# Optimization experiments

Hardware: AMD Instinct MI355X
Metric: run time of the kernel (lower is better)

The kernel has to match this reference:

```python
import jax, jax.numpy as jnp
import numpy as np

N_NODES = 50000
N_EDGES = 800000
IN_DIM = 128
HIDDEN = 64
HEADS = 4
OUT_DIM = 64
NEG_SLOPE = 0.2


def setup_inputs() -> dict:
    key = jax.random.key(0)
    ks = jax.random.split(key, 16)
    def lin(k, fan_in, fan_out):
        return jax.random.normal(k, (fan_in, fan_out), dtype=jnp.float32) * (1.0 / np.sqrt(fan_in))
    def attn(k):
        return jax.random.normal(k, (HEADS, HIDDEN), dtype=jnp.float32) * 0.1
    inp = {
        "x": jax.random.normal(ks[0], (N_NODES, IN_DIM), dtype=jnp.float32),
        "src": jax.random.randint(ks[1], (N_EDGES,), 0, N_NODES, dtype=jnp.int32),
        "dst": jax.random.randint(ks[2], (N_EDGES,), 0, N_NODES, dtype=jnp.int32),
        # layer 0: in_dim -> heads*hidden
        "W0": lin(ks[3], IN_DIM, HEADS * HIDDEN),
        "al0": attn(ks[4]),
        "ar0": attn(ks[5]),
        # layer 1: heads*hidden -> heads*hidden
        "W1": lin(ks[6], HEADS * HIDDEN, HEADS * HIDDEN),
        "al1": attn(ks[7]),
        "ar1": attn(ks[8]),
        # final layer: heads*hidden -> heads*out_dim
        "W2": lin(ks[9], HEADS * HIDDEN, HEADS * OUT_DIM),
        "al2": jax.random.normal(ks[10], (HEADS, OUT_DIM), dtype=jnp.float32) * 0.1,
        "ar2": jax.random.normal(ks[11], (HEADS, OUT_DIM), dtype=jnp.float32) * 0.1,
        # output head: out_dim -> 1
        "Wout": lin(ks[12], OUT_DIM, 1),
        "bout": jnp.zeros((1,), dtype=jnp.float32),
    }
    return inp


def gat_layer(x, src, dst, W, al, ar):
    """DGL-style multi-head graph attention conv (edge gather/softmax/aggregate)."""
    N = x.shape[0]
    H, D = al.shape
    h = (x @ W).reshape(N, H, D)                      # [N,H,D]
    el = jnp.sum(h * al, axis=-1)                     # [N,H]
    er = jnp.sum(h * ar, axis=-1)                     # [N,H]
    e = jax.nn.leaky_relu(el[src] + er[dst], NEG_SLOPE)   # [E,H]
    # numerically-stable edge softmax segmented by destination node
    m = jax.ops.segment_max(e, dst, num_segments=N)   # [N,H]
    m = jnp.where(jnp.isfinite(m), m, 0.0)
    ex = jnp.exp(e - m[dst])                          # [E,H]
    denom = jax.ops.segment_sum(ex, dst, num_segments=N)  # [N,H]
    alpha = ex / (denom[dst] + 1e-9)                  # [E,H]
    msg = h[src] * alpha[..., None]                   # [E,H,D] (dominant traffic)
    out = jax.ops.segment_sum(msg, dst, num_segments=N)   # [N,H,D]
    return jax.nn.elu(out)


def reference(x, src, dst, W0, al0, ar0, W1, al1, ar1, W2, al2, ar2, Wout, bout):
    N = x.shape[0]
    # layer 0 (threshold layer also produces node index split index1/index0)
    h = gat_layer(x, src, dst, W0, al0, ar0)          # [N,H,HID]
    h = h.reshape(N, -1)                              # flatten(start=1,end=2)
    # middle layer
    h = gat_layer(h, src, dst, W1, al1, ar1)
    h = h.reshape(N, -1)
    # final layer + head-mean pool
    feats = gat_layer(h, src, dst, W2, al2, ar2)      # [N,H,OUT]
    feats = feats.mean(axis=1)                        # [N,OUT]
    out = jax.nn.relu(feats @ Wout + bout)            # [N,1]
    return out
```

## Files before the change

### kernel.cpp

```cpp
#include <hip/hip_runtime.h>
#include <hip/hip_fp16.h>
#include <math.h>

#define NN 50000
#define NE 800000
#define HEADS 4
#define HID 64
#define HD 256
#define NEG_SLOPE 0.2f

typedef __attribute__((ext_vector_type(8))) short short8;
typedef __attribute__((ext_vector_type(4))) float f32x4;
typedef __attribute__((ext_vector_type(2))) unsigned int uint2v;

__device__ __forceinline__ unsigned short f2bf(float f) {
    unsigned u = __float_as_uint(f);
    u += 0x7fff + ((u >> 16) & 1);
    return (unsigned short)(u >> 16);
}
__device__ __forceinline__ float bf2f(unsigned short b) {
    return __uint_as_float(((unsigned)b) << 16);
}

__device__ __forceinline__ float h2f_bits(unsigned short b) {
    __half_raw r; r.x = b;
    return __half2float(__half(r));
}
__device__ __forceinline__ unsigned short f2h_bits(float f) {
    __half_raw r(__float2half(f));
    return r.x;
}

__device__ __forceinline__ void wsplit_one(const float* W, unsigned short* Wf, int idx) {
    int lane = idx & 63;
    int tile = (idx >> 6) & 15;
    int kb   = idx >> 10;
    int col  = tile * 16 + (lane & 15);
    int krow = kb * 32 + (lane >> 4) * 8;
    unsigned short* p = Wf + ((size_t)(kb * 16 + tile) * 2 * 64 + lane) * 8;
#pragma unroll
    for (int j = 0; j < 8; j++) {
        float v = W[(size_t)(krow + j) * HD + col];
        unsigned short h = f2bf(v);
        unsigned short l = f2bf(v - bf2f(h));
        p[j] = h;
        p[512 + j] = l;
    }
}

__global__ __launch_bounds__(256) void prep_count_kernel(
    const float* __restrict__ W0, unsigned short* __restrict__ Wf0,
    const float* __restrict__ W1, unsigned short* __restrict__ Wf1,
    const float* __restrict__ W2, unsigned short* __restrict__ Wf2,
    const int* __restrict__ dst, int* __restrict__ cnt) {
    int b = (int)blockIdx.x;
    if (b < 80) {
        int idx = b * 256 + (int)threadIdx.x;
        const int n0 = 4 * 16 * 64;
        const int n1 = 8 * 16 * 64;
        if (idx < n0) wsplit_one(W0, Wf0, idx);
        else if (idx < n0 + n1) wsplit_one(W1, Wf1, idx - n0);
        else if (idx < n0 + 2 * n1) wsplit_one(W2, Wf2, idx - n0 - n1);
    } else {
        int e = ((b - 80) * 256 + (int)threadIdx.x) * 2;
        if (e + 1 < NE) {
            int2 d = *(const int2*)&dst[e];
            atomicAdd(&cnt[d.x], 1);
            atomicAdd(&cnt[d.y], 1);
        } else if (e < NE) {
            atomicAdd(&cnt[dst[e]], 1);
        }
    }
}

__global__ __launch_bounds__(1024) void rowptr_kernel(
    const int* __restrict__ cnt, int* __restrict__ rowptr,
    int* __restrict__ cursor, int n) {
    __shared__ int wsum[16];
    __shared__ int csum_s[16];
    int t = (int)threadIdx.x;
    int base = (int)blockIdx.x * 1024;
    int idx = base + t;
    int lane = t & 63, wid = t >> 6;

    int v = (idx < n) ? cnt[idx] : 0;

    int cp = 0;
    for (int j = t; j < base; j += 1024) cp += cnt[j];

    int x = v;
#pragma unroll
    for (int off = 1; off < 64; off <<= 1) {
        int y = __shfl_up(x, off);
        if (lane >= off) x += y;
    }
#pragma unroll
    for (int off = 32; off > 0; off >>= 1) cp += __shfl_down(cp, off);
    if (lane == 63) wsum[wid] = x;
    if (lane == 0) csum_s[wid] = cp;
    __syncthreads();

    if (t < 16) {
        int wv = wsum[t];
#pragma unroll
        for (int off = 1; off < 16; off <<= 1) {
            int y = __shfl_up(wv, off);
            if (t >= off) wv += y;
        }
        wsum[t] = wv;
    } else if (wid == 1) {
        int cv = (lane < 16) ? csum_s[lane] : 0;
#pragma unroll
        for (int off = 32; off > 0; off >>= 1) cv += __shfl_down(cv, off);
        if (lane == 0) csum_s[0] = cv;
    }
    __syncthreads();

    int waveOff = wid ? wsum[wid - 1] : 0;
    int chunkOff = csum_s[0];
    int incl = x + waveOff + chunkOff;
    int excl = incl - v;
    if (idx < n) { rowptr[idx] = excl; cursor[idx] = excl; }
    if (idx == n - 1) rowptr[n] = incl;
}

template <int K, int F32A>
__device__ __forceinline__ void mfma_gemm_body(
    int bid,
    const ushort* __restrict__ Xh, const ushort* __restrict__ Xl,
    const float* __restrict__ Xf,
    const unsigned short* __restrict__ Wf,
    ushort* __restrict__ H,
    const float* __restrict__ al, const float* __restrict__ ar,
    float* __restrict__ el, float* __restrict__ er,
    ushort* ldsA) {
    constexpr int KB = K / 32;
    int tid = (int)threadIdx.x;
    int w = tid >> 6;
    int lane = tid & 63;
    int rowBase = bid * 64;
    int mrow = lane & 15;
    int q = lane >> 4;

    f32x4 acc[4][4];
#pragma unroll
    for (int r = 0; r < 4; r++)
#pragma unroll
        for (int c = 0; c < 4; c++) {
            f32x4 z = {0.f, 0.f, 0.f, 0.f};
            acc[r][c] = z;
        }

    int srow = tid >> 2, qq = tid & 3;
    int grow = rowBase + srow;
    grow = grow < NN ? grow : NN - 1;
    int sr = srow >> 4, smrow = srow & 15;
    int flane = qq * 16 + smrow;
    ushort* sHi = &ldsA[((size_t)(sr * 2 + 0) * 64 + flane) * 8];

    short8 rh0, rl0, rh1, rl1;
    float4 rf00, rf01, rf10, rf11;

    auto loadA0 = [&](int kb) {
        if constexpr (F32A) {
            const float* xp = Xf + (size_t)grow * K + kb * 32 + qq * 8;
            rf00 = *(const float4*)xp;
            rf01 = *(const float4*)(xp + 4);
        } else {
            rh0 = *(const short8*)(Xh + (size_t)grow * K + kb * 32 + qq * 8);
            rl0 = *(const short8*)(Xl + (size_t)grow * K + kb * 32 + qq * 8);
        }
    };
    auto loadA1 = [&](int kb) {
        if constexpr (F32A) {
            const float* xp = Xf + (size_t)grow * K + kb * 32 + qq * 8;
            rf10 = *(const float4*)xp;
            rf11 = *(const float4*)(xp + 4);
        } else {
            rh1 = *(const short8*)(Xh + (size_t)grow * K + kb * 32 + qq * 8);
            rl1 = *(const short8*)(Xl + (size_t)grow * K + kb * 32 + qq * 8);
        }
    };
    auto cvt8 = [&](float4 a, float4 b, short8& h8, short8& l8) {
        float vv[8] = {a.x, a.y, a.z, a.w, b.x, b.y, b.z, b.w};
#pragma unroll
        for (int j = 0; j < 8; j++) {
            unsigned short hh = f2bf(vv[j]);
            h8[j] = (short)hh;
            l8[j] = (short)f2bf(vv[j] - bf2f(hh));
        }
    };
    auto storeA0 = [&]() {
        if constexpr (F32A) {
            short8 h8, l8;
            cvt8(rf00, rf01, h8, l8);
            *(short8*)sHi = h8;
            *(short8*)(sHi + 512) = l8;
        } else {
            *(short8*)sHi = rh0;
            *(short8*)(sHi + 512) = rl0;
        }
    };
    auto storeA1 = [&]() {
        if constexpr (F32A) {
            short8 h8, l8;
            cvt8(rf10, rf11, h8, l8);
            *(short8*)(sHi + 4096) = h8;
            *(short8*)(sHi + 4096 + 512) = l8;
        } else {
            *(short8*)(sHi + 4096) = rh1;
            *(short8*)(sHi + 4096 + 512) = rl1;
        }
    };

    auto compute = [&](int kb, int pofs) {
        short8 Wh[4], Wl_[4];
#pragma unroll
        for (int c = 0; c < 4; c++) {
            const unsigned short* wp =
                Wf + (((size_t)(kb * 16 + w * 4 + c) * 2) * 64 + lane) * 8;
            Wh[c]  = *(const short8*)wp;
            Wl_[c] = *(const short8*)(wp + 512);
        }
        short8 Ah[4], Al_[4];
#pragma unroll
        for (int r = 0; r < 4; r++) {
            Ah[r]  = *(const short8*)&ldsA[pofs + ((r * 2 + 0) * 64 + lane) * 8];
            Al_[r] = *(const short8*)&ldsA[pofs + ((r * 2 + 1) * 64 + lane) * 8];
        }
#pragma unroll
        for (int c = 0; c < 4; c++)
#pragma unroll
            for (int r = 0; r < 4; r++) {
                acc[r][c] = __builtin_amdgcn_mfma_f32_16x16x32_bf16(Ah[r],  Wh[c],  acc[r][c], 0, 0, 0);
                acc[r][c] = __builtin_amdgcn_mfma_f32_16x16x32_bf16(Ah[r],  Wl_[c], acc[r][c], 0, 0, 0);
                acc[r][c] = __builtin_amdgcn_mfma_f32_16x16x32_bf16(Al_[r], Wh[c],  acc[r][c], 0, 0, 0);
            }
    };

    loadA0(0);
    loadA1(1);
    for (int kb = 0; kb < KB; kb += 2) {
        __syncthreads();
        storeA0();
        storeA1();
        __syncthreads();
        if (kb + 2 < KB) {
            loadA0(kb + 2);
            loadA1(kb + 3);
        }
        compute(kb, 0);
        compute(kb + 1, 4096);
    }

    int n0 = w * 64;
    float alv[4], arv[4];
#pragma unroll
    for (int c = 0; c < 4; c++) {
        alv[c] = al[n0 + c * 16 + mrow];
        arv[c] = ar[n0 + c * 16 + mrow];
    }
#pragma unroll
    for (int r = 0; r < 4; r++) {
        float pl[4] = {0.f, 0.f, 0.f, 0.f};
        float pr[4] = {0.f, 0.f, 0.f, 0.f};
#pragma unroll
        for (int c = 0; c < 4; c++)
#pragma unroll
            for (int g = 0; g < 4; g++) {
                pl[g] += acc[r][c][g] * alv[c];
                pr[g] += acc[r][c][g] * arv[c];
            }
#pragma unroll
        for (int g = 0; g < 4; g++) {
#pragma unroll
            for (int off = 1; off < 16; off <<= 1) {
                pl[g] += __shfl_xor(pl[g], off);
                pr[g] += __shfl_xor(pr[g], off);
            }
        }
#pragma unroll
        for (int g = 0; g < 4; g++) {
            int row = rowBase + r * 16 + q * 4 + g;
            if (row < NN) {
#pragma unroll
                for (int c = 0; c < 4; c++)
                    H[(size_t)row * HD + n0 + c * 16 + mrow] = f2h_bits(acc[r][c][g]);
                if (mrow == 0) {
                    el[row * 4 + w] = pl[g];
                    er[row * 4 + w] = pr[g];
                }
            }
        }
    }
}

template <int K, int F32A>
__global__ __launch_bounds__(256, 3) void mfma_gemm_kernel(
    const ushort* __restrict__ Xh, const ushort* __restrict__ Xl,
    const float* __restrict__ Xf,
    const unsigned short* __restrict__ Wf,
    ushort* __restrict__ H,
    const float* __restrict__ al, const float* __restrict__ ar,
    float* __restrict__ el, float* __restrict__ er) {
    __shared__ ushort ldsA[2 * 8 * 64 * 8];
    mfma_gemm_body<K, F32A>((int)blockIdx.x, Xh, Xl, Xf, Wf, H, al, ar, el, er, ldsA);
}

__global__ __launch_bounds__(256, 3) void gemm0_scatter_kernel(
    const float* __restrict__ Xf, const unsigned short* __restrict__ Wf,
    ushort* __restrict__ H,
    const float* __restrict__ al, const float* __restrict__ ar,
    float* __restrict__ el, float* __restrict__ er,
    const int* __restrict__ src, const int* __restrict__ dst,
    int* __restrict__ cursor, int* __restrict__ csr_src) {
    __shared__ ushort ldsA[2 * 8 * 64 * 8];
    int b = (int)blockIdx.x;
    int g = b / 5, rem = b % 5;
    if (rem == 0) {
        mfma_gemm_body<128, 1>(g, nullptr, nullptr, Xf, Wf, H, al, ar, el, er, ldsA);
    } else {
        int e = (g * 4 + (rem - 1)) * 256 + (int)threadIdx.x;
        if (e < NE) {
            int p = atomicAdd(&cursor[dst[e]], 1);
            csr_src[p] = src[e];
        }
    }
}

__device__ __forceinline__ float lrelu(float x) { return fmaxf(x, NEG_SLOPE * x); }

__device__ __forceinline__ float4 us4tof4(ushort4 u) {
    float4 f;
    f.x = h2f_bits(u.x); f.y = h2f_bits(u.y);
    f.z = h2f_bits(u.z); f.w = h2f_bits(u.w);
    return f;
}

template <int FINAL>
__global__ __launch_bounds__(256) void gat_node_kernel(
    const ushort* __restrict__ H, const float* __restrict__ el, const float* __restrict__ er,
    const int* __restrict__ rowptr, const int* __restrict__ csr_src,
    ushort* __restrict__ out_hi, ushort* __restrict__ out_lo,
    const float* __restrict__ Wout, const float* __restrict__ bout,
    float* __restrict__ final_out) {
    int wave = threadIdx.x >> 6, lane = threadIdx.x & 63;
    int v = blockIdx.x * 4 + wave;
    if (v >= NN) return;
    int beg = rowptr[v], end = rowptr[v + 1];

    int hh = lane >> 4;
    float er_h = er[v * 4 + hh];
    const float* elh = el + hh;
    unsigned lane4 = (unsigned)(lane * 4);

    float ss0 = 0.f, ss1 = 0.f, ss2 = 0.f, ss3 = 0.f;
    float4 a0 = make_float4(0.f, 0.f, 0.f, 0.f);
    float4 a1 = make_float4(0.f, 0.f, 0.f, 0.f);
    float4 a2 = make_float4(0.f, 0.f, 0.f, 0.f);
    float4 a3 = make_float4(0.f, 0.f, 0.f, 0.f);
    {
        int i = beg;
        for (; i + 4 <= end; i += 4) {
            unsigned s0 = (unsigned)csr_src[i];
            unsigned s1 = (unsigned)csr_src[i + 1];
            unsigned s2 = (unsigned)csr_src[i + 2];
            unsigned s3 = (unsigned)csr_src[i + 3];
            ushort4 q0 = *(const ushort4*)(H + ((s0 << 8) + lane4));
            ushort4 q1 = *(const ushort4*)(H + ((s1 << 8) + lane4));
            ushort4 q2 = *(const ushort4*)(H + ((s2 << 8) + lane4));
            ushort4 q3 = *(const ushort4*)(H + ((s3 << 8) + lane4));
            float w0 = __expf(lrelu(elh[s0 * 4u] + er_h));
            float w1 = __expf(lrelu(elh[s1 * 4u] + er_h));
            float w2 = __expf(lrelu(elh[s2 * 4u] + er_h));
            float w3 = __expf(lrelu(elh[s3 * 4u] + er_h));
            float4 h0 = us4tof4(q0);
            float4 h1 = us4tof4(q1);
            float4 h2 = us4tof4(q2);
            float4 h3 = us4tof4(q3);
            ss0 += w0; ss1 += w1; ss2 += w2; ss3 += w3;
            a0.x += w0 * h0.x; a0.y += w0 * h0.y; a0.z += w0 * h0.z; a0.w += w0 * h0.w;
            a1.x += w1 * h1.x; a1.y += w1 * h1.y; a1.z += w1 * h1.z; a1.w += w1 * h1.w;
            a2.x += w2 * h2.x; a2.y += w2 * h2.y; a2.z += w2 * h2.z; a2.w += w2 * h2.w;
            a3.x += w3 * h3.x; a3.y += w3 * h3.y; a3.z += w3 * h3.z; a3.w += w3 * h3.w;
        }
        for (; i < end; i++) {
            unsigned s0 = (unsigned)csr_src[i];
            ushort4 q0 = *(const ushort4*)(H + ((s0 << 8) + lane4));
            float w0 = __expf(lrelu(elh[s0 * 4u] + er_h));
            float4 h0 = us4tof4(q0);
            ss0 += w0;
            a0.x += w0 * h0.x; a0.y += w0 * h0.y; a0.z += w0 * h0.z; a0.w += w0 * h0.w;
        }
    }
    float ssum = (ss0 + ss1) + (ss2 + ss3);
    float4 acc;
    acc.x = (a0.x + a1.x) + (a2.x + a3.x);
    acc.y = (a0.y + a1.y) + (a2.y + a3.y);
    acc.z = (a0.z + a1.z) + (a2.z + a3.z);
    acc.w = (a0.w + a1.w) + (a2.w + a3.w);

    float inv = 1.0f / (ssum + 1e-9f);
    acc.x *= inv; acc.y *= inv; acc.z *= inv; acc.w *= inv;

    acc.x = acc.x > 0.f ? acc.x : expm1f(acc.x);
    acc.y = acc.y > 0.f ? acc.y : expm1f(acc.y);
    acc.z = acc.z > 0.f ? acc.z : expm1f(acc.z);
    acc.w = acc.w > 0.f ? acc.w : expm1f(acc.w);

    if (!FINAL) {
        ushort4 hv, lv;
        hv.x = f2bf(acc.x); lv.x = f2bf(acc.x - bf2f(hv.x));
        hv.y = f2bf(acc.y); lv.y = f2bf(acc.y - bf2f(hv.y));
        hv.z = f2bf(acc.z); lv.z = f2bf(acc.z - bf2f(hv.z));
        hv.w = f2bf(acc.w); lv.w = f2bf(acc.w - bf2f(hv.w));
        uint2v ph = { (unsigned)hv.x | ((unsigned)hv.y << 16),
                      (unsigned)hv.z | ((unsigned)hv.w << 16) };
        uint2v pl = { (unsigned)lv.x | ((unsigned)lv.y << 16),
                      (unsigned)lv.z | ((unsigned)lv.w << 16) };
        __builtin_nontemporal_store(ph, (uint2v*)(out_hi + (size_t)v * HD + lane * 4));
        __builtin_nontemporal_store(pl, (uint2v*)(out_lo + (size_t)v * HD + lane * 4));
    } else {
        acc.x += __shfl_xor(acc.x, 16); acc.x += __shfl_xor(acc.x, 32);
        acc.y += __shfl_xor(acc.y, 16); acc.y += __shfl_xor(acc.y, 32);
        acc.z += __shfl_xor(acc.z, 16); acc.z += __shfl_xor(acc.z, 32);
        acc.w += __shfl_xor(acc.w, 16); acc.w += __shfl_xor(acc.w, 32);
        float4 w4 = *(const float4*)&Wout[(lane & 15) * 4];
        float p = 0.25f * (acc.x * w4.x + acc.y * w4.y + acc.z * w4.z + acc.w * w4.w);
        p += __shfl_xor(p, 1);
        p += __shfl_xor(p, 2);
        p += __shfl_xor(p, 4);
        p += __shfl_xor(p, 8);
        if (lane == 0) final_out[v] = fmaxf(p + bout[0], 0.f);
    }
}

extern "C" void kernel_launch(void* const* d_in, const int* in_sizes, int n_in,
                              void* d_out, int out_size, void* d_ws, size_t ws_size,
                              hipStream_t stream) {
    const float* x    = (const float*)d_in[0];
    const int*   src  = (const int*)d_in[1];
    const int*   dst  = (const int*)d_in[2];
    const float* W0   = (const float*)d_in[3];
    const float* al0  = (const float*)d_in[4];
    const float* ar0  = (const float*)d_in[5];
    const float* W1   = (const float*)d_in[6];
    const float* al1  = (const float*)d_in[7];
    const float* ar1  = (const float*)d_in[8];
    const float* W2   = (const float*)d_in[9];
    const float* al2  = (const float*)d_in[10];
    const float* ar2  = (const float*)d_in[11];
    const float* Wout = (const float*)d_in[12];
    const float* bout = (const float*)d_in[13];
    float* outp = (float*)d_out;

    char* ws = (char*)d_ws;
    size_t off = 0;
    auto carve = [&](size_t n) -> char* {
        char* p = ws + off;
        off += (n + 255) & ~(size_t)255;
        return p;
    };
    ushort* h_buf  = (ushort*)carve((size_t)NN * HD * 2);
    ushort* xh     = (ushort*)carve((size_t)NN * HD * 2);
    ushort* xl     = (ushort*)carve((size_t)NN * HD * 2);
    float*  el     = (float*)carve((size_t)NN * HEADS * 4);
    float*  er     = (float*)carve((size_t)NN * HEADS * 4);
    int*    cnt    = (int*)carve((size_t)NN * 4);
    int*    cursor = (int*)carve((size_t)NN * 4);
    int*    rowptr = (int*)carve((size_t)(NN + 1) * 4);
    int*    csr_src= (int*)carve((size_t)NE * 4);
    unsigned short* Wf0 = (unsigned short*)carve((size_t)4 * 16 * 64 * 16 * 2);
    unsigned short* Wf1 = (unsigned short*)carve((size_t)8 * 16 * 64 * 16 * 2);
    unsigned short* Wf2 = (unsigned short*)carve((size_t)8 * 16 * 64 * 16 * 2);

    const int nCountBlk = (NE / 2 + 255) / 256;
    const int gGemm = (NN + 63) / 64;
    const int gNode = (NN + 3) / 4;
    const int NCH = (NN + 1023) / 1024;

    hipMemsetAsync(cnt, 0, (size_t)NN * 4, stream);
    prep_count_kernel<<<80 + nCountBlk, 256, 0, stream>>>(W0, Wf0, W1, Wf1, W2, Wf2, dst, cnt);
    rowptr_kernel<<<NCH, 1024, 0, stream>>>(cnt, rowptr, cursor, NN);
    gemm0_scatter_kernel<<<gGemm * 5, 256, 0, stream>>>(
        x, Wf0, h_buf, al0, ar0, el, er, src, dst, cursor, csr_src);
    gat_node_kernel<0><<<gNode, 256, 0, stream>>>(h_buf, el, er, rowptr, csr_src,
                                                  xh, xl, nullptr, nullptr, nullptr);
    mfma_gemm_kernel<256, 0><<<gGemm, 256, 0, stream>>>(xh, xl, nullptr, Wf1,
                                                        h_buf, al1, ar1, el, er);
    gat_node_kernel<0><<<gNode, 256, 0, stream>>>(h_buf, el, er, rowptr, csr_src,
                                                  xh, xl, nullptr, nullptr, nullptr);
    mfma_gemm_kernel<256, 0><<<gGemm, 256, 0, stream>>>(xh, xl, nullptr, Wf2,
                                                        h_buf, al2, ar2, el, er);
    gat_node_kernel<1><<<gNode, 256, 0, stream>>>(h_buf, el, er, rowptr, csr_src,
                                                  nullptr, nullptr, Wout, bout, outp);
}
```

Measured before the change: 451.1 us.

## Stage full-K activation tile in LDS once for layer-1/2 GEMMs

Replaces the double-buffered K-loop GEMM for the 256-wide hidden layers with a kernel that loads the whole 64x256 hi/lo bf16 activation tile into LDS up front, syncs once, then runs all K steps without further barriers. This removes the per-iteration syncthreads and the register staging of the loop. In exchange the block uses 64 KB of LDS and more registers, so occupancy drops (launch bounds changes from 3 to 2 blocks) and load latency is no longer overlapped with compute. The shared epilogue is factored into a helper.

```diff
diff --git a/kernel.cpp b/kernel.cpp
--- a/kernel.cpp
+++ b/kernel.cpp
@@ -124,16 +124,61 @@
     if (idx == n - 1) rowptr[n] = incl;
 }
 
-template <int K, int F32A>
-__device__ __forceinline__ void mfma_gemm_body(
+__device__ __forceinline__ void gemm_epilogue(
+    f32x4 (&acc)[4][4], int rowBase, int w, int mrow, int q,
+    ushort* __restrict__ H, const float* __restrict__ al, const float* __restrict__ ar,
+    float* __restrict__ el, float* __restrict__ er) {
+    int n0 = w * 64;
+    float alv[4], arv[4];
+#pragma unroll
+    for (int c = 0; c < 4; c++) {
+        alv[c] = al[n0 + c * 16 + mrow];
+        arv[c] = ar[n0 + c * 16 + mrow];
+    }
+#pragma unroll
+    for (int r = 0; r < 4; r++) {
+        float pl[4] = {0.f, 0.f, 0.f, 0.f};
+        float pr[4] = {0.f, 0.f, 0.f, 0.f};
+#pragma unroll
+        for (int c = 0; c < 4; c++)
+#pragma unroll
+            for (int g = 0; g < 4; g++) {
+                pl[g] += acc[r][c][g] * alv[c];
+                pr[g] += acc[r][c][g] * arv[c];
+            }
+#pragma unroll
+        for (int g = 0; g < 4; g++) {
+#pragma unroll
+            for (int off = 1; off < 16; off <<= 1) {
+                pl[g] += __shfl_xor(pl[g], off);
+                pr[g] += __shfl_xor(pr[g], off);
+            }
+        }
+#pragma unroll
+        for (int g = 0; g < 4; g++) {
+            int row = rowBase + r * 16 + q * 4 + g;
+            if (row < NN) {
+#pragma unroll
+                for (int c = 0; c < 4; c++)
+                    H[(size_t)row * HD + n0 + c * 16 + mrow] = f2h_bits(acc[r][c][g]);
+                if (mrow == 0) {
+                    el[row * 4 + w] = pl[g];
+                    er[row * 4 + w] = pr[g];
+                }
+            }
+        }
+    }
+}
+
+__device__ __forceinline__ void mfma_gemm_body_f32(
     int bid,
-    const ushort* __restrict__ Xh, const ushort* __restrict__ Xl,
     const float* __restrict__ Xf,
     const unsigned short* __restrict__ Wf,
     ushort* __restrict__ H,
     const float* __restrict__ al, const float* __restrict__ ar,
     float* __restrict__ el, float* __restrict__ er,
     ushort* ldsA) {
+    constexpr int K = 128;
     constexpr int KB = K / 32;
     int tid = (int)threadIdx.x;
     int w = tid >> 6;
@@ -158,28 +203,17 @@
     int flane = qq * 16 + smrow;
     ushort* sHi = &ldsA[((size_t)(sr * 2 + 0) * 64 + flane) * 8];
 
-    short8 rh0, rl0, rh1, rl1;
     float4 rf00, rf01, rf10, rf11;
 
     auto loadA0 = [&](int kb) {
-        if constexpr (F32A) {
-            const float* xp = Xf + (size_t)grow * K + kb * 32 + qq * 8;
-            rf00 = *(const float4*)xp;
-            rf01 = *(const float4*)(xp + 4);
-        } else {
-            rh0 = *(const short8*)(Xh + (size_t)grow * K + kb * 32 + qq * 8);
-            rl0 = *(const short8*)(Xl + (size_t)grow * K + kb * 32 + qq * 8);
-        }
+        const float* xp = Xf + (size_t)grow * K + kb * 32 + qq * 8;
+        rf00 = *(const float4*)xp;
+        rf01 = *(const float4*)(xp + 4);
     };
     auto loadA1 = [&](int kb) {
-        if constexpr (F32A) {
-            const float* xp = Xf + (size_t)grow * K + kb * 32 + qq * 8;
-            rf10 = *(const float4*)xp;
-            rf11 = *(const float4*)(xp + 4);
-        } else {
-            rh1 = *(const short8*)(Xh + (size_t)grow * K + kb * 32 + qq * 8);
-            rl1 = *(const short8*)(Xl + (size_t)grow * K + kb * 32 + qq * 8);
-        }
+        const float* xp = Xf + (size_t)grow * K + kb * 32 + qq * 8;
+        rf10 = *(const float4*)xp;
+        rf11 = *(const float4*)(xp + 4);
     };
     auto cvt8 = [&](float4 a, float4 b, short8& h8, short8& l8) {
         float vv[8] = {a.x, a.y, a.z, a.w, b.x, b.y, b.z, b.w};
@@ -191,26 +225,16 @@
         }
     };
     auto storeA0 = [&]() {
-        if constexpr (F32A) {
-            short8 h8, l8;
-            cvt8(rf00, rf01, h8, l8);
-            *(short8*)sHi = h8;
-            *(short8*)(sHi + 512) = l8;
-        } else {
-            *(short8*)sHi = rh0;
-            *(short8*)(sHi + 512) = rl0;
-        }
+        short8 h8, l8;
+        cvt8(rf00, rf01, h8, l8);
+        *(short8*)sHi = h8;
+        *(short8*)(sHi + 512) = l8;
     };
     auto storeA1 = [&]() {
-        if constexpr (F32A) {
-            short8 h8, l8;
-            cvt8(rf10, rf11, h8, l8);
-            *(short8*)(sHi + 4096) = h8;
-            *(short8*)(sHi + 4096 + 512) = l8;
-        } else {
-            *(short8*)(sHi + 4096) = rh1;
-            *(short8*)(sHi + 4096 + 512) = rl1;
-        }
+        short8 h8, l8;
+        cvt8(rf10, rf11, h8, l8);
+        *(short8*)(sHi + 4096) = h8;
+        *(short8*)(sHi + 4096 + 512) = l8;
     };
 
     auto compute = [&](int kb, int pofs) {
@@ -253,58 +277,7 @@
         compute(kb + 1, 4096);
     }
 
-    int n0 = w * 64;
-    float alv[4], arv[4];
-#pragma unroll
-    for (int c = 0; c < 4; c++) {
-        alv[c] = al[n0 + c * 16 + mrow];
-        arv[c] = ar[n0 + c * 16 + mrow];
-    }
-#pragma unroll
-    for (int r = 0; r < 4; r++) {
-        float pl[4] = {0.f, 0.f, 0.f, 0.f};
-        float pr[4] = {0.f, 0.f, 0.f, 0.f};
-#pragma unroll
-        for (int c = 0; c < 4; c++)
-#pragma unroll
-            for (int g = 0; g < 4; g++) {
-                pl[g] += acc[r][c][g] * alv[c];
-                pr[g] += acc[r][c][g] * arv[c];
-            }
-#pragma unroll
-        for (int g = 0; g < 4; g++) {
-#pragma unroll
-            for (int off = 1; off < 16; off <<= 1) {
-                pl[g] += __shfl_xor(pl[g], off);
-                pr[g] += __shfl_xor(pr[g], off);
-            }
-        }
-#pragma unroll
-        for (int g = 0; g < 4; g++) {
-            int row = rowBase + r * 16 + q * 4 + g;
-            if (row < NN) {
-#pragma unroll
-                for (int c = 0; c < 4; c++)
-                    H[(size_t)row * HD + n0 + c * 16 + mrow] = f2h_bits(acc[r][c][g]);
-                if (mrow == 0) {
-                    el[row * 4 + w] = pl[g];
-                    er[row * 4 + w] = pr[g];
-                }
-            }
-        }
-    }
-}
-
-template <int K, int F32A>
-__global__ __launch_bounds__(256, 3) void mfma_gemm_kernel(
-    const ushort* __restrict__ Xh, const ushort* __restrict__ Xl,
-    const float* __restrict__ Xf,
-    const unsigned short* __restrict__ Wf,
-    ushort* __restrict__ H,
-    const float* __restrict__ al, const float* __restrict__ ar,
-    float* __restrict__ el, float* __restrict__ er) {
-    __shared__ ushort ldsA[2 * 8 * 64 * 8];
-    mfma_gemm_body<K, F32A>((int)blockIdx.x, Xh, Xl, Xf, Wf, H, al, ar, el, er, ldsA);
+    gemm_epilogue(acc, rowBase, w, mrow, q, H, al, ar, el, er);
 }
 
 __global__ __launch_bounds__(256, 3) void gemm0_scatter_kernel(
@@ -318,7 +291,7 @@
     int b = (int)blockIdx.x;
     int g = b / 5, rem = b % 5;
     if (rem == 0) {
-        mfma_gemm_body<128, 1>(g, nullptr, nullptr, Xf, Wf, H, al, ar, el, er, ldsA);
+        mfma_gemm_body_f32(g, Xf, Wf, H, al, ar, el, er, ldsA);
     } else {
         int e = (g * 4 + (rem - 1)) * 256 + (int)threadIdx.x;
         if (e < NE) {
@@ -326,6 +299,81 @@
             csr_src[p] = src[e];
         }
     }
+}
+
+__global__ __launch_bounds__(256, 2) void mfma_gemm_fullk_kernel(
+    const ushort* __restrict__ Xh, const ushort* __restrict__ Xl,
+    const unsigned short* __restrict__ Wf,
+    ushort* __restrict__ H,
+    const float* __restrict__ al, const float* __restrict__ ar,
+    float* __restrict__ el, float* __restrict__ er) {
+    constexpr int K = 256;
+    constexpr int KB = K / 32;
+    __shared__ ushort ldsA[KB * 4 * 2 * 64 * 8];
+    int tid = (int)threadIdx.x;
+    int w = tid >> 6;
+    int lane = tid & 63;
+    int rowBase = (int)blockIdx.x * 64;
+    int mrow = lane & 15;
+    int q = lane >> 4;
+
+    int srow = tid >> 2, qq = tid & 3;
+    int grow = rowBase + srow;
+    grow = grow < NN ? grow : NN - 1;
+    int sr = srow >> 4, smrow = srow & 15;
+    int flane = qq * 16 + smrow;
+    const ushort* xhp = Xh + (size_t)grow * K + qq * 8;
+    const ushort* xlp = Xl + (size_t)grow * K + qq * 8;
+
+    short8 sh[KB], sl[KB];
+#pragma unroll
+    for (int kb = 0; kb < KB; kb++) {
+        sh[kb] = *(const short8*)(xhp + kb * 32);
+        sl[kb] = *(const short8*)(xlp + kb * 32);
+    }
+#pragma unroll
+    for (int kb = 0; kb < KB; kb++) {
+        *(short8*)&ldsA[((size_t)(kb * 8 + sr * 2 + 0) * 64 + flane) * 8] = sh[kb];
+        *(short8*)&ldsA[((size_t)(kb * 8 + sr * 2 + 1) * 64 + flane) * 8] = sl[kb];
+    }
+    __syncthreads();
+
+    f32x4 acc[4][4];
+#pragma unroll
+    for (int r = 0; r < 4; r++)
+#pragma unroll
+        for (int c = 0; c < 4; c++) {
+            f32x4 z = {0.f, 0.f, 0.f, 0.f};
+            acc[r][c] = z;
+        }
+
+    for (int kb = 0; kb < KB; kb++) {
+        const ushort* Abase = &ldsA[(size_t)kb * 8 * 512];
+        short8 Wh[4], Wl_[4];
+#pragma unroll
+        for (int c = 0; c < 4; c++) {
+            const unsigned short* wp =
+                Wf + (((size_t)(kb * 16 + w * 4 + c) * 2) * 64 + lane) * 8;
+            Wh[c]  = *(const short8*)wp;
+            Wl_[c] = *(const short8*)(wp + 512);
+        }
+        short8 Ah[4], Al_[4];
+#pragma unroll
+        for (int r = 0; r < 4; r++) {
+            Ah[r]  = *(const short8*)&Abase[((r * 2 + 0) * 64 + lane) * 8];
+            Al_[r] = *(const short8*)&Abase[((r * 2 + 1) * 64 + lane) * 8];
+        }
+#pragma unroll
+        for (int c = 0; c < 4; c++)
+#pragma unroll
+            for (int r = 0; r < 4; r++) {
+                acc[r][c] = __builtin_amdgcn_mfma_f32_16x16x32_bf16(Ah[r],  Wh[c],  acc[r][c], 0, 0, 0);
+                acc[r][c] = __builtin_amdgcn_mfma_f32_16x16x32_bf16(Ah[r],  Wl_[c], acc[r][c], 0, 0, 0);
+                acc[r][c] = __builtin_amdgcn_mfma_f32_16x16x32_bf16(Al_[r], Wh[c],  acc[r][c], 0, 0, 0);
+            }
+    }
+
+    gemm_epilogue(acc, rowBase, w, mrow, q, H, al, ar, el, er);
 }
 
 __device__ __forceinline__ float lrelu(float x) { return fmaxf(x, NEG_SLOPE * x); }
@@ -486,12 +534,12 @@
         x, Wf0, h_buf, al0, ar0, el, er, src, dst, cursor, csr_src);
     gat_node_kernel<0><<<gNode, 256, 0, stream>>>(h_buf, el, er, rowptr, csr_src,
                                                   xh, xl, nullptr, nullptr, nullptr);
-    mfma_gemm_kernel<256, 0><<<gGemm, 256, 0, stream>>>(xh, xl, nullptr, Wf1,
-                                                        h_buf, al1, ar1, el, er);
+    mfma_gemm_fullk_kernel<<<gGemm, 256, 0, stream>>>(xh, xl, Wf1,
+                                                      h_buf, al1, ar1, el, er);
     gat_node_kernel<0><<<gNode, 256, 0, stream>>>(h_buf, el, er, rowptr, csr_src,
                                                   xh, xl, nullptr, nullptr, nullptr);
-    mfma_gemm_kernel<256, 0><<<gGemm, 256, 0, stream>>>(xh, xl, nullptr, Wf2,
-                                                        h_buf, al2, ar2, el, er);
+    mfma_gemm_fullk_kernel<<<gGemm, 256, 0, stream>>>(xh, xl, Wf2,
+                                                      h_buf, al2, ar2, el, er);
     gat_node_kernel<1><<<gNode, 256, 0, stream>>>(h_buf, el, er, rowptr, csr_src,
                                                   nullptr, nullptr, Wout, bout, outp);
 }
```

Result: no change. 445.9 us (-1.1%).
